# Kernel tuning notes

Measured on AMD Instinct MI355X. Metric: run time of the kernel, lower is better.

## Reference

```python
import jax, jax.numpy as jnp
import numpy as np

B, S, IN, H, L, HEM, HTR = 128, 256, 88, 400, 100, 100, 200


def _lin(x, W, b):
    return x @ W.T + b


def setup_inputs() -> dict:
    key = jax.random.key(0)
    ks = iter(jax.random.split(key, 64))
    def p(shape, scale=0.05):
        return jax.random.normal(next(ks), shape, dtype=jnp.float32) * scale
    inp = {
        "x": jax.random.uniform(next(ks), (B, S, IN), dtype=jnp.float32),
        # bidirectional tanh RNN (1 layer)
        "Wih_f": p((H, IN)), "Whh_f": p((H, H)), "bih_f": p((H,)), "bhh_f": p((H,)),
        "Wih_b": p((H, IN)), "Whh_b": p((H, H)), "bih_b": p((H,)), "bhh_b": p((H,)),
        # DKS combiner
        "Wc": p((H, L)), "bc": p((H,)),
        "Wmu": p((L, H)), "bmu": p((L,)),
        "Wsig": p((L, H)), "bsig": p((L,)),
        # emission MLP
        "We1": p((HEM, L)), "be1": p((HEM,)),
        "We2": p((HEM, HEM)), "be2": p((HEM,)),
        "We3": p((IN, HEM)), "be3": p((IN,)),
        # gate G
        "Wg1": p((HTR, L)), "bg1": p((HTR,)),
        "Wg2": p((L, HTR)), "bg2": p((L,)),
        # proposed mean H
        "Wh1": p((HTR, L)), "bh1": p((HTR,)),
        "Wh2": p((L, HTR)), "bh2": p((L,)),
        # gated linear mu (init: identity weight, zero bias)
        "Wmg": jnp.eye(L, dtype=jnp.float32), "bmg": jnp.zeros((L,), jnp.float32),
        "Wsg": p((L, L)), "bsg": p((L,)),
        # pre-drawn sampling noise (stands in for torch.randn_like)
        "noise_inf": jax.random.normal(next(ks), (S, B, L), dtype=jnp.float32),
        "z0_gen": jax.random.normal(next(ks), (B, L), dtype=jnp.float32),
        "noise_gen": jax.random.normal(next(ks), (S, B, L), dtype=jnp.float32),
    }
    return inp


def _forward(x, Wih_f, Whh_f, bih_f, bhh_f, Wih_b, Whh_b, bih_b, bhh_b,
             Wc, bc, Wmu, bmu, Wsig, bsig,
             We1, be1, We2, be2, We3, be3,
             Wg1, bg1, Wg2, bg2, Wh1, bh1, Wh2, bh2, Wmg, bmg, Wsg, bsg,
             noise_inf, z0_gen, noise_gen):
    Bs = x.shape[0]
    # ---- bidirectional tanh RNN (batch_first) ----
    xf = (x @ Wih_f.T + bih_f).transpose(1, 0, 2)  # [S,B,H]
    xb = (x @ Wih_b.T + bih_b).transpose(1, 0, 2)

    def rnn_step_f(h, xt):
        h = jnp.tanh(xt + h @ Whh_f.T + bhh_f)
        return h, h

    def rnn_step_b(h, xt):
        h = jnp.tanh(xt + h @ Whh_b.T + bhh_b)
        return h, h

    h0 = jnp.zeros((Bs, H), x.dtype)
    _, out_f = jax.lax.scan(rnn_step_f, h0, xf)                 # [S,B,H] forward dir
    _, out_b_rev = jax.lax.scan(rnn_step_b, h0, xb[::-1])       # backward dir
    h_right = out_b_rev[::-1]                                   # [S,B,H], time-aligned
    # (h_left = out_f unused for combiner_type='dks')

    # ---- DKS combiner: sequential latent sampling ----
    def comb_step(z_prev, inp):
        hr_t, n_t = inp
        h = 0.5 * (jnp.tanh(z_prev @ Wc.T + bc) + hr_t)
        mu = h @ Wmu.T + bmu
        var = jax.nn.softplus(h @ Wsig.T + bsig)
        z_t = mu + jnp.sqrt(var) * n_t
        return z_t, (z_t, mu, var)

    z0 = jnp.zeros((Bs, L), x.dtype)
    _, (Z, mus_inf, sigmas_inf) = jax.lax.scan(comb_step, z0, (h_right, noise_inf))
    Z = Z.transpose(1, 0, 2)                 # [B,S,L]
    mus_inf = mus_inf.transpose(1, 0, 2)
    sigmas_inf = sigmas_inf.transpose(1, 0, 2)

    # ---- decoder emission (vectorized over B,S) ----
    e = jax.nn.relu(_lin(Z, We1, be1))
    e = jax.nn.relu(_lin(e, We2, be2))
    x_hat = jax.nn.sigmoid(_lin(e, We3, be3))  # [B,S,IN]

    # ---- decoder transition prior (sequential, self-driven) ----
    def tr_step(z_prev, n_t):
        g = jax.nn.sigmoid(jax.nn.relu(z_prev @ Wg1.T + bg1) @ Wg2.T + bg2)
        h_prop = jax.nn.relu(z_prev @ Wh1.T + bh1) @ Wh2.T + bh2
        mu = h_prop * g + (z_prev @ Wmg.T + bmg) * (1.0 - g)
        sigma = jax.nn.softplus(jax.nn.relu(h_prop) @ Wsg.T + bsg)
        z_t = mu + jnp.sqrt(sigma) * n_t
        return z_t, (mu, sigma)

    _, (mus_gen, sigmas_gen) = jax.lax.scan(tr_step, z0_gen, noise_gen)
    mus_gen = mus_gen.transpose(1, 0, 2)
    sigmas_gen = sigmas_gen.transpose(1, 0, 2)

    return (x_hat, mus_inf, sigmas_inf, mus_gen, sigmas_gen)


def reference(x, Wih_f, Whh_f, bih_f, bhh_f, Wih_b, Whh_b, bih_b, bhh_b,
              Wc, bc, Wmu, bmu, Wsig, bsig,
              We1, be1, We2, be2, We3, be3,
              Wg1, bg1, Wg2, bg2, Wh1, bh1, Wh2, bh2, Wmg, bmg, Wsg, bsg,
              noise_inf, z0_gen, noise_gen):
    return _forward(x, Wih_f, Whh_f, bih_f, bhh_f, Wih_b, Whh_b, bih_b, bhh_b,
                    Wc, bc, Wmu, bmu, Wsig, bsig,
                    We1, be1, We2, be2, We3, be3,
                    Wg1, bg1, Wg2, bg2, Wh1, bh1, Wh2, bh2, Wmg, bmg, Wsg, bsg,
                    noise_inf, z0_gen, noise_gen)
```

## Files before the change

### kernel.cpp

```cpp
#include <hip/hip_runtime.h>
#include <math.h>

typedef float f32x4 __attribute__((ext_vector_type(4)));
typedef short s16x8 __attribute__((ext_vector_type(8)));
typedef unsigned short u16;

#define DI __device__ __forceinline__

DI float bf2f(u16 h) { union { unsigned u; float f; } v; v.u = ((unsigned)h) << 16; return v.f; }
DI u16 f2bf(float f) {
  union { float f; unsigned u; } v; v.f = f;
  unsigned u = v.u;
  u += 0x7FFFu + ((u >> 16) & 1u);
  return (u16)(u >> 16);
}
DI float tanh_fast(float x) {
  float e = __expf(2.f * x);
  return 1.f - 2.f / (e + 1.f);
}
DI float sigmoid_f(float x) { return 1.f / (1.f + __expf(-x)); }
DI float softplus_f(float x) { return fmaxf(x, 0.f) + log1pf(__expf(-fabsf(x))); }
DI f32x4 mfma16(s16x8 a, s16x8 b, f32x4 c) {
  return __builtin_amdgcn_mfma_f32_16x16x32_bf16(a, b, c, 0, 0, 0);
}
DI void bar_lds() { asm volatile("s_waitcnt lgkmcnt(0)\n\ts_barrier" ::: "memory"); }
DI int fa(int k, int row) { return ((k >> 5) << 9) + ((((k >> 3) & 3) * 16 + row) << 3) + (k & 7); }

union P16 { uint4 v[2]; u16 u[16]; };

static constexpr size_t U_RNN = 0;
static constexpr size_t U_C1  = 186368;
static constexpr size_t U_C2  = 243712;
static constexpr size_t U_GA  = 336896;
static constexpr size_t U_GB  = 394240;
static constexpr size_t U_GC  = 444416;
static constexpr size_t U_E1  = 473088;
static constexpr size_t U_E2  = 487424;
static constexpr size_t U_E3  = 501760;
static constexpr size_t U_IN  = 514048;
static constexpr size_t U_SL  = 552448;

__global__ void k_pack(u16* __restrict__ ws,
    const float* __restrict__ Whh_b, const float* __restrict__ Wc,
    const float* __restrict__ Wmu, const float* __restrict__ Wsig,
    const float* __restrict__ Wg1, const float* __restrict__ Wh1,
    const float* __restrict__ Wg2, const float* __restrict__ Wh2,
    const float* __restrict__ Wmg, const float* __restrict__ Wsg,
    const float* __restrict__ We1, const float* __restrict__ We2,
    const float* __restrict__ We3, const float* __restrict__ Wih_b)
{
  int r = blockIdx.x, l = threadIdx.x;
  int region, local;
  if      (r < 364)  { region = 0; local = r; }
  else if (r < 476)  { region = 1; local = r - 364; }
  else if (r < 658)  { region = 2; local = r - 476; }
  else if (r < 770)  { region = 3; local = r - 658; }
  else if (r < 868)  { region = 4; local = r - 770; }
  else if (r < 924)  { region = 5; local = r - 868; }
  else if (r < 952)  { region = 6; local = r - 924; }
  else if (r < 980)  { region = 7; local = r - 952; }
  else if (r < 1004) { region = 8; local = r - 980; }
  else               { region = 9; local = r - 1004; }

  int NT; size_t base;
  switch (region) {
    case 0: NT = 28; base = U_RNN; break;
    case 1: NT = 28; base = U_C1;  break;
    case 2: NT = 14; base = U_C2;  break;
    case 3: NT = 28; base = U_GA;  break;
    case 4: NT = 14; base = U_GB;  break;
    case 5: NT = 14; base = U_GC;  break;
    case 6: NT = 7;  base = U_E1;  break;
    case 7: NT = 7;  base = U_E2;  break;
    case 8: NT = 6;  base = U_E3;  break;
    default:NT = 25; base = U_IN;  break;
  }
  int kt = local / NT, nt = local % NT;
  u16* out = ws + base + ((size_t)local * 64 + l) * 8;
  #pragma unroll
  for (int e = 0; e < 8; ++e) {
    int k = kt * 32 + (l >> 4) * 8 + e;
    int n = nt * 16 + (l & 15);
    float v = 0.f;
    switch (region) {
      case 0: if (n < 400 && k < 400) v = Whh_b[n * 400 + k]; break;
      case 1: if (n < 400 && k < 100) v = Wc[n * 100 + k]; break;
      case 2: if (n < 112) { if (n < 100 && k < 400) v = Wmu[n * 400 + k]; }
              else { int m = n - 112; if (m < 100 && k < 400) v = Wsig[m * 400 + k]; } break;
      case 3: if (n < 208) { if (n < 200 && k < 100) v = Wg1[n * 100 + k]; }
              else if (n < 416) { int m = n - 208; if (m < 200 && k < 100) v = Wh1[m * 100 + k]; } break;
      case 4: if (n < 112) { if (n < 100 && k < 200) v = Wg2[n * 200 + k]; }
              else { int m = n - 112; if (m < 100 && k < 200) v = Wh2[m * 200 + k]; } break;
      case 5: if (n < 112) { if (n < 100 && k < 100) v = Wmg[n * 100 + k]; }
              else { int m = n - 112; if (m < 100 && k < 100) v = Wsg[m * 100 + k]; } break;
      case 6: if (n < 100 && k < 100) v = We1[n * 100 + k]; break;
      case 7: if (n < 100 && k < 100) v = We2[n * 100 + k]; break;
      case 8: if (n < 88  && k < 100) v = We3[n * 100 + k]; break;
      default:if (n < 400 && k < 88)  v = Wih_b[n * 88 + k]; break;
    }
    out[e] = f2bf(v);
  }
}

__global__ __launch_bounds__(256) void k_proj(
    const float* __restrict__ x, const float* __restrict__ bih_b,
    const u16* __restrict__ pk_in, u16* __restrict__ slot)
{
  __shared__ __align__(16) u16 x_lds[16][104];
  const int tid = threadIdx.x;
  const int cblk = blockIdx.x;
  const int b = cblk >> 4, s0 = (cblk & 15) << 4;
  const float* xg = x + (size_t)cblk * 16 * 88;
  for (int idx = tid; idx < 16 * 104; idx += 256) {
    int r = idx / 104, k = idx % 104;
    x_lds[r][k] = (k < 88) ? f2bf(xg[r * 88 + k]) : (u16)0;
  }
  __syncthreads();
  const int w = tid >> 6, l = tid & 63, g = l >> 4, li = l & 15;
  const int bid2 = b >> 4, r2 = b & 15, g2 = r2 >> 2, q2 = r2 & 3;
  s16x8 a[3];
  #pragma unroll
  for (int kt = 0; kt < 3; ++kt)
    a[kt] = *(const s16x8*)&x_lds[li][kt * 32 + g * 8];
  for (int nt = w; nt < 25; nt += 4) {
    f32x4 acc = (f32x4){0.f, 0.f, 0.f, 0.f};
    #pragma unroll
    for (int kt = 0; kt < 3; ++kt) {
      s16x8 bfr = *(const s16x8*)(pk_in + ((size_t)(kt * 25 + nt) * 64 + l) * 8);
      acc = mfma16(a[kt], bfr, acc);
    }
    int i = nt * 16 + li;
    float bias = bih_b[i];
    int thr = ((i >> 6) << 6) + (g2 << 4) + (i & 15);
    int elem = (((i >> 4) & 3) << 2) + q2;
    #pragma unroll
    for (int q = 0; q < 4; ++q) {
      int s = s0 + g * 4 + q;
      slot[((size_t)(s * 8 + bid2) * 448 + thr) * 16 + elem] = f2bf(acc[q] + bias);
    }
  }
}

__global__ __launch_bounds__(448) void k_scan(
    const u16* __restrict__ pk_rnn, const u16* __restrict__ pk_c1, const u16* __restrict__ pk_c2,
    const u16* __restrict__ pk_gA, const u16* __restrict__ pk_gB, const u16* __restrict__ pk_gC,
    u16* __restrict__ slot, const float* __restrict__ bhh_b,
    const float* __restrict__ bc, const float* __restrict__ bmu, const float* __restrict__ bsig,
    const float* __restrict__ noise_inf,
    const float* __restrict__ z0g, const float* __restrict__ bg1, const float* __restrict__ bh1,
    const float* __restrict__ bg2, const float* __restrict__ bh2,
    const float* __restrict__ bmg, const float* __restrict__ bsg,
    const float* __restrict__ noise_gen,
    float* __restrict__ mui, float* __restrict__ sgi,
    float* __restrict__ mug, float* __restrict__ sgg)
{
  __shared__ __align__(16) u16 sm[56320];
  const int tid = threadIdx.x;
  const int w = tid >> 6, l = tid & 63, g = l >> 4, li = l & 15;
  const int bid = blockIdx.x;

  {
    uint4 z4 = (uint4){0, 0, 0, 0};
    uint4* p = (uint4*)sm;
    for (int idx = tid; idx < 7040; idx += 448) p[idx] = z4;
  }
  __syncthreads();

  if (bid < 8) {
    const int b0 = bid * 16;
    {
      u16* slab = sm;
      u16* hbuf = sm + 43008;
      {
        const uint4* src = (const uint4*)(pk_rnn + (size_t)10 * 28 * 512);
        uint4* dst = (uint4*)slab;
        for (int idx = tid; idx < 5376; idx += 448) dst[idx] = src[idx];
      }
      s16x8 wf[4][10];
      #pragma unroll
      for (int nt_l = 0; nt_l < 4; ++nt_l) {
        int nt = w * 4 + nt_l;
        #pragma unroll
        for (int kt = 0; kt < 10; ++kt)
          wf[nt_l][kt] = *(const s16x8*)(pk_rnn + ((size_t)(kt * 28 + nt) * 64 + l) * 8);
      }
      bool nv[4]; float bias_r[4];
      #pragma unroll
      for (int nt_l = 0; nt_l < 4; ++nt_l) {
        int n = (w * 4 + nt_l) * 16 + li;
        nv[nt_l] = (n < 400);
        bias_r[nt_l] = nv[nt_l] ? bhh_b[n] : 0.f;
      }
      P16 pf;
      {
        size_t base = ((size_t)(255 * 8 + bid) * 448 + w * 64 + l) * 16;
        pf.v[0] = *(const uint4*)(slot + base);
        pf.v[1] = *(const uint4*)(slot + base + 8);
      }
      __syncthreads();
      int cur = 0;
      for (int t = 0; t < 256; ++t) {
        const int tt = 255 - t;
        f32x4 acc[4];
        #pragma unroll
        for (int i = 0; i < 4; ++i) acc[i] = (f32x4){0.f, 0.f, 0.f, 0.f};
        const u16* hb = hbuf + cur * 6656;
        #pragma unroll
        for (int kt = 0; kt < 13; ++kt) {
          s16x8 a = *(const s16x8*)(hb + kt * 512 + l * 8);
          if (kt < 10) {
            #pragma unroll
            for (int nt_l = 0; nt_l < 4; ++nt_l) acc[nt_l] = mfma16(a, wf[nt_l][kt], acc[nt_l]);
          } else {
            #pragma unroll
            for (int nt_l = 0; nt_l < 4; ++nt_l) {
              s16x8 bfr = *(const s16x8*)(slab + ((size_t)((kt - 10) * 28 + w * 4 + nt_l) * 512) + l * 8);
              acc[nt_l] = mfma16(a, bfr, acc[nt_l]);
            }
          }
        }
        u16* hn = hbuf + (cur ^ 1) * 6656;
        P16 st; st.v[0] = (uint4){0,0,0,0}; st.v[1] = (uint4){0,0,0,0};
        #pragma unroll
        for (int nt_l = 0; nt_l < 4; ++nt_l) {
          if (nv[nt_l]) {
            int n = (w * 4 + nt_l) * 16 + li;
            #pragma unroll
            for (int q = 0; q < 4; ++q) {
              float v = acc[nt_l][q] + bf2f(pf.u[nt_l * 4 + q]) + bias_r[nt_l];
              u16 hv = f2bf(tanh_fast(v));
              hn[fa(n, 4 * g + q)] = hv;
              st.u[nt_l * 4 + q] = hv;
            }
          }
        }
        {
          size_t base = ((size_t)(tt * 8 + bid) * 448 + w * 64 + l) * 16;
          *(uint4*)(slot + base) = st.v[0];
          *(uint4*)(slot + base + 8) = st.v[1];
        }
        if (t < 255) {
          size_t nb = ((size_t)((tt - 1) * 8 + bid) * 448 + w * 64 + l) * 16;
          pf.v[0] = *(const uint4*)(slot + nb);
          pf.v[1] = *(const uint4*)(slot + nb + 8);
        }
        bar_lds();
        cur ^= 1;
      }
    }
    __syncthreads();
    {
      u16* hbF = sm;
      u16* zbF = sm + 6656;
      for (int idx = tid; idx < 8704; idx += 448) sm[idx] = 0;
      s16x8 wC1[4][4], wMu[13], wSg[13];
      #pragma unroll
      for (int nt_l = 0; nt_l < 4; ++nt_l) {
        int nt = w * 4 + nt_l;
        #pragma unroll
        for (int kt = 0; kt < 4; ++kt)
          wC1[nt_l][kt] = *(const s16x8*)(pk_c1 + ((size_t)(kt * 28 + nt) * 64 + l) * 8);
      }
      #pragma unroll
      for (int kt = 0; kt < 13; ++kt) {
        wMu[kt] = *(const s16x8*)(pk_c2 + ((size_t)(kt * 14 + w) * 64 + l) * 8);
        wSg[kt] = *(const s16x8*)(pk_c2 + ((size_t)(kt * 14 + 7 + w) * 64 + l) * 8);
      }
      const int c = w * 16 + li;
      const bool cv = (c < 100);
      const float bmu_c = cv ? bmu[c] : 0.f;
      const float bsig_c = cv ? bsig[c] : 0.f;
      bool nv[4]; float bc_r[4];
      #pragma unroll
      for (int nt_l = 0; nt_l < 4; ++nt_l) {
        int n = (w * 4 + nt_l) * 16 + li;
        nv[nt_l] = (n < 400);
        bc_r[nt_l] = nv[nt_l] ? bc[n] : 0.f;
      }
      P16 pf;
      {
        size_t base = ((size_t)(0 * 8 + bid) * 448 + w * 64 + l) * 16;
        pf.v[0] = *(const uint4*)(slot + base);
        pf.v[1] = *(const uint4*)(slot + base + 8);
      }
      float pf_nz[4];
      #pragma unroll
      for (int q = 0; q < 4; ++q)
        pf_nz[q] = cv ? noise_inf[((size_t)0 * 128 + b0 + g * 4 + q) * 100 + c] : 0.f;
      __syncthreads();

      for (int t = 0; t < 256; ++t) {
        {
          s16x8 az[4];
          #pragma unroll
          for (int kt = 0; kt < 4; ++kt)
            az[kt] = *(const s16x8*)(zbF + kt * 512 + l * 8);
          f32x4 a1[4];
          #pragma unroll
          for (int i = 0; i < 4; ++i) a1[i] = (f32x4){0.f, 0.f, 0.f, 0.f};
          #pragma unroll
          for (int kt = 0; kt < 4; ++kt) {
            #pragma unroll
            for (int nt_l = 0; nt_l < 4; ++nt_l) a1[nt_l] = mfma16(az[kt], wC1[nt_l][kt], a1[nt_l]);
          }
          #pragma unroll
          for (int nt_l = 0; nt_l < 4; ++nt_l) {
            if (nv[nt_l]) {
              int n = (w * 4 + nt_l) * 16 + li;
              #pragma unroll
              for (int q = 0; q < 4; ++q) {
                float hv = 0.5f * (tanh_fast(a1[nt_l][q] + bc_r[nt_l]) + bf2f(pf.u[nt_l * 4 + q]));
                hbF[fa(n, 4 * g + q)] = f2bf(hv);
              }
            }
          }
          if (t < 255) {
            size_t nb = ((size_t)((t + 1) * 8 + bid) * 448 + w * 64 + l) * 16;
            pf.v[0] = *(const uint4*)(slot + nb);
            pf.v[1] = *(const uint4*)(slot + nb + 8);
          }
        }
        bar_lds();
        {
          f32x4 am = (f32x4){0.f,0.f,0.f,0.f}, as_ = am;
          #pragma unroll
          for (int kt = 0; kt < 13; ++kt) {
            s16x8 a = *(const s16x8*)(hbF + kt * 512 + l * 8);
            am = mfma16(a, wMu[kt], am);
            as_ = mfma16(a, wSg[kt], as_);
          }
          #pragma unroll
          for (int q = 0; q < 4; ++q) {
            int r = g * 4 + q;
            float mu = am[q] + bmu_c;
            float va = softplus_f(as_[q] + bsig_c);
            if (cv) {
              size_t o = ((size_t)(b0 + r) * 256 + t) * 100 + c;
              mui[o] = mu;
              sgi[o] = va;
              float z = mu + sqrtf(va) * pf_nz[q];
              zbF[fa(c, r)] = f2bf(z);
              slot[(size_t)(t * 8 + bid) * 7168 + r * 112 + c] = f2bf(z);
            }
          }
          if (t < 255) {
            #pragma unroll
            for (int q = 0; q < 4; ++q)
              if (cv) pf_nz[q] = noise_inf[((size_t)(t + 1) * 128 + b0 + g * 4 + q) * 100 + c];
          }
        }
        bar_lds();
      }
    }
  } else {
    const int b0 = (bid - 8) * 16;
    u16* zbF  = sm;
    u16* rhbF = sm + 2048;
    u16* t1F  = sm + 4096;
    u16* t2F  = sm + 7680;
    for (int idx = tid; idx < 2048; idx += 448) {
      int r = idx >> 7, c = idx & 127;
      zbF[fa(c, r)] = (c < 100) ? f2bf(z0g[(b0 + r) * 100 + c]) : (u16)0;
    }
    s16x8 wA[4][4], wBg[7], wBh[7], wCm[4], wCs[4];
    #pragma unroll
    for (int nt_l = 0; nt_l < 4; ++nt_l) {
      int nt = w * 4 + nt_l;
      #pragma unroll
      for (int kt = 0; kt < 4; ++kt)
        wA[nt_l][kt] = *(const s16x8*)(pk_gA + ((size_t)(kt * 28 + nt) * 64 + l) * 8);
    }
    #pragma unroll
    for (int kt = 0; kt < 7; ++kt) {
      wBg[kt] = *(const s16x8*)(pk_gB + ((size_t)(kt * 14 + w) * 64 + l) * 8);
      wBh[kt] = *(const s16x8*)(pk_gB + ((size_t)(kt * 14 + 7 + w) * 64 + l) * 8);
    }
    #pragma unroll
    for (int kt = 0; kt < 4; ++kt) {
      wCm[kt] = *(const s16x8*)(pk_gC + ((size_t)(kt * 14 + w) * 64 + l) * 8);
      wCs[kt] = *(const s16x8*)(pk_gC + ((size_t)(kt * 14 + 7 + w) * 64 + l) * 8);
    }
    const int c = w * 16 + li;
    const bool cv = (c < 100);
    const float bg2_c = cv ? bg2[c] : 0.f;
    const float bh2_c = cv ? bh2[c] : 0.f;
    const float bmg_c = cv ? bmg[c] : 0.f;
    const float bsg_c = cv ? bsg[c] : 0.f;
    float b1r[4];
    #pragma unroll
    for (int nt_l = 0; nt_l < 4; ++nt_l) {
      int n = (w * 4 + nt_l) * 16 + li;
      bool is1 = n < 208;
      int j = is1 ? n : n - 208;
      b1r[nt_l] = (n < 416 && j < 200) ? (is1 ? bg1[j] : bh1[j]) : 0.f;
    }
    float pfn[4];
    #pragma unroll
    for (int q = 0; q < 4; ++q)
      pfn[q] = cv ? noise_gen[((size_t)0 * 128 + b0 + g * 4 + q) * 100 + c] : 0.f;
    __syncthreads();

    for (int t = 0; t < 256; ++t) {
      s16x8 az[4];
      #pragma unroll
      for (int kt = 0; kt < 4; ++kt)
        az[kt] = *(const s16x8*)(zbF + kt * 512 + l * 8);
      {
        f32x4 a1[4];
        #pragma unroll
        for (int i = 0; i < 4; ++i) a1[i] = (f32x4){0.f, 0.f, 0.f, 0.f};
        #pragma unroll
        for (int kt = 0; kt < 4; ++kt) {
          #pragma unroll
          for (int nt_l = 0; nt_l < 4; ++nt_l) a1[nt_l] = mfma16(az[kt], wA[nt_l][kt], a1[nt_l]);
        }
        #pragma unroll
        for (int nt_l = 0; nt_l < 4; ++nt_l) {
          int n = (w * 4 + nt_l) * 16 + li;
          if (n < 416) {
            bool is1 = n < 208;
            int j = is1 ? n : n - 208;
            u16* dst = is1 ? t1F : t2F;
            #pragma unroll
            for (int q = 0; q < 4; ++q)
              dst[fa(j, 4 * g + q)] = f2bf(fmaxf(a1[nt_l][q] + b1r[nt_l], 0.f));
          }
        }
      }
      bar_lds();
      float muq[4];
      {
        f32x4 ag = (f32x4){0.f,0.f,0.f,0.f}, ah = ag, am = ag;
        #pragma unroll
        for (int kt = 0; kt < 7; ++kt) {
          s16x8 x1 = *(const s16x8*)(t1F + kt * 512 + l * 8);
          ag = mfma16(x1, wBg[kt], ag);
        }
        #pragma unroll
        for (int kt = 0; kt < 7; ++kt) {
          s16x8 x2 = *(const s16x8*)(t2F + kt * 512 + l * 8);
          ah = mfma16(x2, wBh[kt], ah);
        }
        #pragma unroll
        for (int kt = 0; kt < 4; ++kt) am = mfma16(az[kt], wCm[kt], am);
        #pragma unroll
        for (int q = 0; q < 4; ++q) {
          int r = g * 4 + q;
          float gv = sigmoid_f(ag[q] + bg2_c);
          float hp = ah[q] + bh2_c;
          float m0 = am[q] + bmg_c;
          muq[q] = hp * gv + m0 * (1.f - gv);
          rhbF[fa(c, r)] = f2bf(fmaxf(hp, 0.f));
          if (cv) mug[((size_t)(b0 + r) * 256 + t) * 100 + c] = muq[q];
        }
      }
      bar_lds();
      {
        f32x4 as2 = (f32x4){0.f,0.f,0.f,0.f};
        #pragma unroll
        for (int kt = 0; kt < 4; ++kt) {
          s16x8 xr = *(const s16x8*)(rhbF + kt * 512 + l * 8);
          as2 = mfma16(xr, wCs[kt], as2);
        }
        #pragma unroll
        for (int q = 0; q < 4; ++q) {
          int r = g * 4 + q;
          float sg = softplus_f(as2[q] + bsg_c);
          if (cv) {
            sgg[((size_t)(b0 + r) * 256 + t) * 100 + c] = sg;
            zbF[fa(c, r)] = f2bf(muq[q] + sqrtf(sg) * pfn[q]);
          }
        }
        if (t < 255) {
          #pragma unroll
          for (int q = 0; q < 4; ++q)
            if (cv) pfn[q] = noise_gen[((size_t)(t + 1) * 128 + b0 + g * 4 + q) * 100 + c];
        }
      }
      bar_lds();
    }
  }
}

__global__ __launch_bounds__(448) void k_dec(
    const u16* __restrict__ slot,
    const u16* __restrict__ pk_e1, const u16* __restrict__ pk_e2, const u16* __restrict__ pk_e3,
    const float* __restrict__ be1, const float* __restrict__ be2, const float* __restrict__ be3,
    float* __restrict__ xh)
{
  __shared__ __align__(16) u16 sm[3 * 2176];
  u16* zb = sm; u16* e1b = sm + 2176; u16* e2b = sm + 4352;
  const int tid = threadIdx.x;
  const int w = tid >> 6, l = tid & 63, g = l >> 4, li = l & 15;
  const int cc = blockIdx.x;
  const int b = cc >> 4, s0 = (cc & 15) << 4;
  const int bid2 = b >> 4, r2 = b & 15;

  s16x8 w1[4], w2[4], w3[4];
  #pragma unroll
  for (int kt = 0; kt < 4; ++kt) {
    w1[kt] = *(const s16x8*)(pk_e1 + ((size_t)(kt * 7 + w) * 64 + l) * 8);
    w2[kt] = *(const s16x8*)(pk_e2 + ((size_t)(kt * 7 + w) * 64 + l) * 8);
    if (w < 6) w3[kt] = *(const s16x8*)(pk_e3 + ((size_t)(kt * 6 + w) * 64 + l) * 8);
  }
  {
    for (int idx = tid; idx < 224; idx += 448) {
      int r = idx / 14, cj = idx % 14;
      size_t src = ((size_t)((s0 + r) * 8 + bid2)) * 7168 + r2 * 112 + cj * 8;
      *(uint4*)(zb + r * 136 + cj * 8) = *(const uint4*)(slot + src);
    }
    for (int idx = tid; idx < 3 * 384; idx += 448) {
      int bi = idx / 384, j = idx % 384;
      (sm + bi * 2176)[(j / 24) * 136 + 112 + (j % 24)] = 0;
    }
  }
  __syncthreads();
  const int c = w * 16 + li;
  {
    f32x4 acc = (f32x4){0.f,0.f,0.f,0.f};
    #pragma unroll
    for (int kt = 0; kt < 4; ++kt) {
      s16x8 a = *(const s16x8*)(zb + li * 136 + kt * 32 + g * 8);
      acc = mfma16(a, w1[kt], acc);
    }
    float bias = (c < 100) ? be1[c] : 0.f;
    #pragma unroll
    for (int q = 0; q < 4; ++q)
      e1b[(g * 4 + q) * 136 + c] = f2bf(fmaxf(acc[q] + bias, 0.f));
  }
  bar_lds();
  {
    f32x4 acc = (f32x4){0.f,0.f,0.f,0.f};
    #pragma unroll
    for (int kt = 0; kt < 4; ++kt) {
      s16x8 a = *(const s16x8*)(e1b + li * 136 + kt * 32 + g * 8);
      acc = mfma16(a, w2[kt], acc);
    }
    float bias = (c < 100) ? be2[c] : 0.f;
    #pragma unroll
    for (int q = 0; q < 4; ++q)
      e2b[(g * 4 + q) * 136 + c] = f2bf(fmaxf(acc[q] + bias, 0.f));
  }
  bar_lds();
  if (w < 6) {
    f32x4 acc = (f32x4){0.f,0.f,0.f,0.f};
    #pragma unroll
    for (int kt = 0; kt < 4; ++kt) {
      s16x8 a = *(const s16x8*)(e2b + li * 136 + kt * 32 + g * 8);
      acc = mfma16(a, w3[kt], acc);
    }
    int n = w * 16 + li;
    if (n < 88) {
      float bias = be3[n];
      #pragma unroll
      for (int q = 0; q < 4; ++q)
        xh[((size_t)b * 256 + s0 + g * 4 + q) * 88 + n] = sigmoid_f(acc[q] + bias);
    }
  }
}

extern "C" void kernel_launch(void* const* d_in, const int* in_sizes, int n_in,
                              void* d_out, int out_size, void* d_ws, size_t ws_size,
                              hipStream_t stream) {
  const float* x      = (const float*)d_in[0];
  const float* Wih_b  = (const float*)d_in[5];
  const float* Whh_b  = (const float*)d_in[6];
  const float* bih_b  = (const float*)d_in[7];
  const float* bhh_b  = (const float*)d_in[8];
  const float* Wc     = (const float*)d_in[9];
  const float* bc     = (const float*)d_in[10];
  const float* Wmu    = (const float*)d_in[11];
  const float* bmu    = (const float*)d_in[12];
  const float* Wsig   = (const float*)d_in[13];
  const float* bsig   = (const float*)d_in[14];
  const float* We1    = (const float*)d_in[15];
  const float* be1    = (const float*)d_in[16];
  const float* We2    = (const float*)d_in[17];
  const float* be2    = (const float*)d_in[18];
  const float* We3    = (const float*)d_in[19];
  const float* be3    = (const float*)d_in[20];
  const float* Wg1    = (const float*)d_in[21];
  const float* bg1    = (const float*)d_in[22];
  const float* Wg2    = (const float*)d_in[23];
  const float* bg2    = (const float*)d_in[24];
  const float* Wh1    = (const float*)d_in[25];
  const float* bh1    = (const float*)d_in[26];
  const float* Wh2    = (const float*)d_in[27];
  const float* bh2    = (const float*)d_in[28];
  const float* Wmg    = (const float*)d_in[29];
  const float* bmg    = (const float*)d_in[30];
  const float* Wsg    = (const float*)d_in[31];
  const float* bsg    = (const float*)d_in[32];
  const float* noise_inf = (const float*)d_in[33];
  const float* z0_gen    = (const float*)d_in[34];
  const float* noise_gen = (const float*)d_in[35];

  u16* ws16 = (u16*)d_ws;
  float* out = (float*)d_out;
  float* xh  = out;
  float* mui = out + 2883584;
  float* sgi = out + 6160384;
  float* mug = out + 9437184;
  float* sgg = out + 12713984;
  u16* slot = ws16 + U_SL;

  k_pack<<<1079, 64, 0, stream>>>(ws16, Whh_b, Wc, Wmu, Wsig, Wg1, Wh1, Wg2, Wh2,
                                  Wmg, Wsg, We1, We2, We3, Wih_b);
  k_proj<<<2048, 256, 0, stream>>>(x, bih_b, ws16 + U_IN, slot);
  k_scan<<<16, 448, 0, stream>>>(ws16 + U_RNN, ws16 + U_C1, ws16 + U_C2,
                                 ws16 + U_GA, ws16 + U_GB, ws16 + U_GC,
                                 slot, bhh_b,
                                 bc, bmu, bsig, noise_inf,
                                 z0_gen, bg1, bh1, bg2, bh2, bmg, bsg, noise_gen,
                                 mui, sgi, mug, sgg);
  k_dec<<<2048, 448, 0, stream>>>(slot, ws16 + U_E1, ws16 + U_E2, ws16 + U_E3,
                                  be1, be2, be3, xh);
}
```

Before: 1.775 ms.

## Hold full backward RNN weights in registers and skip padded MFMA tiles

The backward RNN scan now keeps all 13 K-tiles of its recurrent weight in registers instead of staging the last three tiles in an LDS slab. That removes per-step LDS weight reads and shrinks shared memory from about 110KB to 32KB. MFMAs and weight loads are also skipped for column tiles that are pure padding (beyond 25 or 26 tiles). The LDS hidden-state write is moved after the global slot store. The catch is much higher register pressure, roughly 208 VGPRs for the weight fragments alone, which could cause spills.

Measured after the change: 4.252 ms. 2.4x slower.

```diff
diff --git a/kernel.cpp b/kernel.cpp
--- a/kernel.cpp
+++ b/kernel.cpp
@@ -154,7 +154,7 @@
     float* __restrict__ mui, float* __restrict__ sgi,
     float* __restrict__ mug, float* __restrict__ sgg)
 {
-  __shared__ __align__(16) u16 sm[56320];
+  __shared__ __align__(16) u16 sm[16384];
   const int tid = threadIdx.x;
   const int w = tid >> 6, l = tid & 63, g = l >> 4, li = l & 15;
   const int bid = blockIdx.x;
@@ -162,34 +162,29 @@
   {
     uint4 z4 = (uint4){0, 0, 0, 0};
     uint4* p = (uint4*)sm;
-    for (int idx = tid; idx < 7040; idx += 448) p[idx] = z4;
+    for (int idx = tid; idx < 2048; idx += 448) p[idx] = z4;
   }
   __syncthreads();
 
   if (bid < 8) {
     const int b0 = bid * 16;
     {
-      u16* slab = sm;
-      u16* hbuf = sm + 43008;
-      {
-        const uint4* src = (const uint4*)(pk_rnn + (size_t)10 * 28 * 512);
-        uint4* dst = (uint4*)slab;
-        for (int idx = tid; idx < 5376; idx += 448) dst[idx] = src[idx];
-      }
-      s16x8 wf[4][10];
+      u16* hbuf = sm;
+      s16x8 wf[4][13];
       #pragma unroll
       for (int nt_l = 0; nt_l < 4; ++nt_l) {
         int nt = w * 4 + nt_l;
-        #pragma unroll
-        for (int kt = 0; kt < 10; ++kt)
-          wf[nt_l][kt] = *(const s16x8*)(pk_rnn + ((size_t)(kt * 28 + nt) * 64 + l) * 8);
-      }
-      bool nv[4]; float bias_r[4];
+        if (nt < 25) {
+          #pragma unroll
+          for (int kt = 0; kt < 13; ++kt)
+            wf[nt_l][kt] = *(const s16x8*)(pk_rnn + ((size_t)(kt * 28 + nt) * 64 + l) * 8);
+        }
+      }
+      float bias_r[4];
       #pragma unroll
       for (int nt_l = 0; nt_l < 4; ++nt_l) {
-        int n = (w * 4 + nt_l) * 16 + li;
-        nv[nt_l] = (n < 400);
-        bias_r[nt_l] = nv[nt_l] ? bhh_b[n] : 0.f;
+        int nt = w * 4 + nt_l;
+        bias_r[nt_l] = (nt < 25) ? bhh_b[nt * 16 + li] : 0.f;
       }
       P16 pf;
       {
@@ -208,29 +203,18 @@
         #pragma unroll
         for (int kt = 0; kt < 13; ++kt) {
           s16x8 a = *(const s16x8*)(hb + kt * 512 + l * 8);
-          if (kt < 10) {
-            #pragma unroll
-            for (int nt_l = 0; nt_l < 4; ++nt_l) acc[nt_l] = mfma16(a, wf[nt_l][kt], acc[nt_l]);
-          } else {
-            #pragma unroll
-            for (int nt_l = 0; nt_l < 4; ++nt_l) {
-              s16x8 bfr = *(const s16x8*)(slab + ((size_t)((kt - 10) * 28 + w * 4 + nt_l) * 512) + l * 8);
-              acc[nt_l] = mfma16(a, bfr, acc[nt_l]);
-            }
-          }
-        }
-        u16* hn = hbuf + (cur ^ 1) * 6656;
+          #pragma unroll
+          for (int nt_l = 0; nt_l < 4; ++nt_l)
+            if (w * 4 + nt_l < 25) acc[nt_l] = mfma16(a, wf[nt_l][kt], acc[nt_l]);
+        }
         P16 st; st.v[0] = (uint4){0,0,0,0}; st.v[1] = (uint4){0,0,0,0};
         #pragma unroll
         for (int nt_l = 0; nt_l < 4; ++nt_l) {
-          if (nv[nt_l]) {
-            int n = (w * 4 + nt_l) * 16 + li;
+          if (w * 4 + nt_l < 25) {
             #pragma unroll
             for (int q = 0; q < 4; ++q) {
               float v = acc[nt_l][q] + bf2f(pf.u[nt_l * 4 + q]) + bias_r[nt_l];
-              u16 hv = f2bf(tanh_fast(v));
-              hn[fa(n, 4 * g + q)] = hv;
-              st.u[nt_l * 4 + q] = hv;
+              st.u[nt_l * 4 + q] = f2bf(tanh_fast(v));
             }
           }
         }
@@ -238,6 +222,16 @@
           size_t base = ((size_t)(tt * 8 + bid) * 448 + w * 64 + l) * 16;
           *(uint4*)(slot + base) = st.v[0];
           *(uint4*)(slot + base + 8) = st.v[1];
+        }
+        u16* hn = hbuf + (cur ^ 1) * 6656;
+        #pragma unroll
+        for (int nt_l = 0; nt_l < 4; ++nt_l) {
+          if (w * 4 + nt_l < 25) {
+            int n = (w * 4 + nt_l) * 16 + li;
+            #pragma unroll
+            for (int q = 0; q < 4; ++q)
+              hn[fa(n, 4 * g + q)] = st.u[nt_l * 4 + q];
+          }
         }
         if (t < 255) {
           size_t nb = ((size_t)((tt - 1) * 8 + bid) * 448 + w * 64 + l) * 16;
@@ -257,9 +251,11 @@
       #pragma unroll
       for (int nt_l = 0; nt_l < 4; ++nt_l) {
         int nt = w * 4 + nt_l;
-        #pragma unroll
-        for (int kt = 0; kt < 4; ++kt)
-          wC1[nt_l][kt] = *(const s16x8*)(pk_c1 + ((size_t)(kt * 28 + nt) * 64 + l) * 8);
+        if (nt < 25) {
+          #pragma unroll
+          for (int kt = 0; kt < 4; ++kt)
+            wC1[nt_l][kt] = *(const s16x8*)(pk_c1 + ((size_t)(kt * 28 + nt) * 64 + l) * 8);
+        }
       }
       #pragma unroll
       for (int kt = 0; kt < 13; ++kt) {
@@ -270,12 +266,11 @@
       const bool cv = (c < 100);
       const float bmu_c = cv ? bmu[c] : 0.f;
       const float bsig_c = cv ? bsig[c] : 0.f;
-      bool nv[4]; float bc_r[4];
+      float bc_r[4];
       #pragma unroll
       for (int nt_l = 0; nt_l < 4; ++nt_l) {
-        int n = (w * 4 + nt_l) * 16 + li;
-        nv[nt_l] = (n < 400);
-        bc_r[nt_l] = nv[nt_l] ? bc[n] : 0.f;
+        int nt = w * 4 + nt_l;
+        bc_r[nt_l] = (nt < 25) ? bc[nt * 16 + li] : 0.f;
       }
       P16 pf;
       {
@@ -301,11 +296,12 @@
           #pragma unroll
           for (int kt = 0; kt < 4; ++kt) {
             #pragma unroll
-            for (int nt_l = 0; nt_l < 4; ++nt_l) a1[nt_l] = mfma16(az[kt], wC1[nt_l][kt], a1[nt_l]);
+            for (int nt_l = 0; nt_l < 4; ++nt_l)
+              if (w * 4 + nt_l < 25) a1[nt_l] = mfma16(az[kt], wC1[nt_l][kt], a1[nt_l]);
           }
           #pragma unroll
           for (int nt_l = 0; nt_l < 4; ++nt_l) {
-            if (nv[nt_l]) {
+            if (w * 4 + nt_l < 25) {
               int n = (w * 4 + nt_l) * 16 + li;
               #pragma unroll
               for (int q = 0; q < 4; ++q) {
@@ -366,9 +362,11 @@
     #pragma unroll
     for (int nt_l = 0; nt_l < 4; ++nt_l) {
       int nt = w * 4 + nt_l;
-      #pragma unroll
-      for (int kt = 0; kt < 4; ++kt)
-        wA[nt_l][kt] = *(const s16x8*)(pk_gA + ((size_t)(kt * 28 + nt) * 64 + l) * 8);
+      if (nt < 26) {
+        #pragma unroll
+        for (int kt = 0; kt < 4; ++kt)
+          wA[nt_l][kt] = *(const s16x8*)(pk_gA + ((size_t)(kt * 28 + nt) * 64 + l) * 8);
+      }
     }
     #pragma unroll
     for (int kt = 0; kt < 7; ++kt) {
@@ -412,7 +410,8 @@
         #pragma unroll
         for (int kt = 0; kt < 4; ++kt) {
           #pragma unroll
-          for (int nt_l = 0; nt_l < 4; ++nt_l) a1[nt_l] = mfma16(az[kt], wA[nt_l][kt], a1[nt_l]);
+          for (int nt_l = 0; nt_l < 4; ++nt_l)
+            if (w * 4 + nt_l < 26) a1[nt_l] = mfma16(az[kt], wA[nt_l][kt], a1[nt_l]);
         }
         #pragma unroll
         for (int nt_l = 0; nt_l < 4; ++nt_l) {
```

## Trim padded MFMA tiles in scan, fold RNN bias into projection, use packed bf16 converts

Applied to the files above, without the earlier changes.

Folds the bhh bias into the input projection kernel so the serial RNN step no longer adds it. In the recurrent scans, the last wave skips MFMA and epilogue work on padded output tiles (wave 6 handles one real tile instead of four; two in the gate stage). Float-to-bf16 rounding now uses the hardware v_cvt_pk_bf16_f32 instruction, and the RNN loop is unrolled by two so the ping-pong buffer pointers are fixed. These cut per-step latency on the serial critical path. The cost is extra code paths split by wave index, plus a possible small rounding difference from summing the two biases before the bf16 store.

After: 2.248 ms. 1.27x slower.

```diff
diff --git a/kernel.cpp b/kernel.cpp
--- a/kernel.cpp
+++ b/kernel.cpp
@@ -4,6 +4,7 @@
 typedef float f32x4 __attribute__((ext_vector_type(4)));
 typedef short s16x8 __attribute__((ext_vector_type(8)));
 typedef unsigned short u16;
+typedef unsigned int u32;
 
 #define DI __device__ __forceinline__
 
@@ -14,6 +15,11 @@
   u += 0x7FFFu + ((u >> 16) & 1u);
   return (u16)(u >> 16);
 }
+DI u32 cvt_pk(float lo, float hi) {
+  u32 r;
+  asm volatile("v_cvt_pk_bf16_f32 %0, %1, %2" : "=v"(r) : "v"(lo), "v"(hi));
+  return r;
+}
 DI float tanh_fast(float x) {
   float e = __expf(2.f * x);
   return 1.f - 2.f / (e + 1.f);
@@ -26,7 +32,7 @@
 DI void bar_lds() { asm volatile("s_waitcnt lgkmcnt(0)\n\ts_barrier" ::: "memory"); }
 DI int fa(int k, int row) { return ((k >> 5) << 9) + ((((k >> 3) & 3) * 16 + row) << 3) + (k & 7); }
 
-union P16 { uint4 v[2]; u16 u[16]; };
+union P16 { uint4 v[2]; u32 w32[8]; u16 u[16]; };
 
 static constexpr size_t U_RNN = 0;
 static constexpr size_t U_C1  = 186368;
@@ -103,7 +109,7 @@
 }
 
 __global__ __launch_bounds__(256) void k_proj(
-    const float* __restrict__ x, const float* __restrict__ bih_b,
+    const float* __restrict__ x, const float* __restrict__ bih_b, const float* __restrict__ bhh_b,
     const u16* __restrict__ pk_in, u16* __restrict__ slot)
 {
   __shared__ __align__(16) u16 x_lds[16][104];
@@ -130,7 +136,7 @@
       acc = mfma16(a[kt], bfr, acc);
     }
     int i = nt * 16 + li;
-    float bias = bih_b[i];
+    float bias = bih_b[i] + bhh_b[i];
     int thr = ((i >> 6) << 6) + (g2 << 4) + (i & 15);
     int elem = (((i >> 4) & 3) << 2) + q2;
     #pragma unroll
@@ -144,7 +150,7 @@
 __global__ __launch_bounds__(448) void k_scan(
     const u16* __restrict__ pk_rnn, const u16* __restrict__ pk_c1, const u16* __restrict__ pk_c2,
     const u16* __restrict__ pk_gA, const u16* __restrict__ pk_gB, const u16* __restrict__ pk_gC,
-    u16* __restrict__ slot, const float* __restrict__ bhh_b,
+    u16* __restrict__ slot,
     const float* __restrict__ bc, const float* __restrict__ bmu, const float* __restrict__ bsig,
     const float* __restrict__ noise_inf,
     const float* __restrict__ z0g, const float* __restrict__ bg1, const float* __restrict__ bh1,
@@ -184,13 +190,6 @@
         for (int kt = 0; kt < 10; ++kt)
           wf[nt_l][kt] = *(const s16x8*)(pk_rnn + ((size_t)(kt * 28 + nt) * 64 + l) * 8);
       }
-      bool nv[4]; float bias_r[4];
-      #pragma unroll
-      for (int nt_l = 0; nt_l < 4; ++nt_l) {
-        int n = (w * 4 + nt_l) * 16 + li;
-        nv[nt_l] = (n < 400);
-        bias_r[nt_l] = nv[nt_l] ? bhh_b[n] : 0.f;
-      }
       P16 pf;
       {
         size_t base = ((size_t)(255 * 8 + bid) * 448 + w * 64 + l) * 16;
@@ -198,54 +197,69 @@
         pf.v[1] = *(const uint4*)(slot + base + 8);
       }
       __syncthreads();
-      int cur = 0;
-      for (int t = 0; t < 256; ++t) {
+
+      auto step = [&](const u16* hb, u16* hn, int t) {
         const int tt = 255 - t;
         f32x4 acc[4];
         #pragma unroll
         for (int i = 0; i < 4; ++i) acc[i] = (f32x4){0.f, 0.f, 0.f, 0.f};
-        const u16* hb = hbuf + cur * 6656;
-        #pragma unroll
-        for (int kt = 0; kt < 13; ++kt) {
-          s16x8 a = *(const s16x8*)(hb + kt * 512 + l * 8);
-          if (kt < 10) {
-            #pragma unroll
-            for (int nt_l = 0; nt_l < 4; ++nt_l) acc[nt_l] = mfma16(a, wf[nt_l][kt], acc[nt_l]);
-          } else {
-            #pragma unroll
-            for (int nt_l = 0; nt_l < 4; ++nt_l) {
-              s16x8 bfr = *(const s16x8*)(slab + ((size_t)((kt - 10) * 28 + w * 4 + nt_l) * 512) + l * 8);
-              acc[nt_l] = mfma16(a, bfr, acc[nt_l]);
+        if (w < 6) {
+          #pragma unroll
+          for (int kt = 0; kt < 13; ++kt) {
+            s16x8 a = *(const s16x8*)(hb + kt * 512 + l * 8);
+            if (kt < 10) {
+              #pragma unroll
+              for (int nt_l = 0; nt_l < 4; ++nt_l) acc[nt_l] = mfma16(a, wf[nt_l][kt], acc[nt_l]);
+            } else {
+              #pragma unroll
+              for (int nt_l = 0; nt_l < 4; ++nt_l) {
+                s16x8 bfr = *(const s16x8*)(slab + ((size_t)((kt - 10) * 28 + w * 4 + nt_l) * 512) + l * 8);
+                acc[nt_l] = mfma16(a, bfr, acc[nt_l]);
+              }
             }
           }
-        }
-        u16* hn = hbuf + (cur ^ 1) * 6656;
+        } else {
+          #pragma unroll
+          for (int kt = 0; kt < 13; ++kt) {
+            s16x8 a = *(const s16x8*)(hb + kt * 512 + l * 8);
+            if (kt < 10) acc[0] = mfma16(a, wf[0][kt], acc[0]);
+            else {
+              s16x8 bfr = *(const s16x8*)(slab + ((size_t)((kt - 10) * 28 + w * 4) * 512) + l * 8);
+              acc[0] = mfma16(a, bfr, acc[0]);
+            }
+          }
+        }
+        const int nvmax = (w < 6) ? 4 : 1;
         P16 st; st.v[0] = (uint4){0,0,0,0}; st.v[1] = (uint4){0,0,0,0};
-        #pragma unroll
-        for (int nt_l = 0; nt_l < 4; ++nt_l) {
-          if (nv[nt_l]) {
-            int n = (w * 4 + nt_l) * 16 + li;
-            #pragma unroll
-            for (int q = 0; q < 4; ++q) {
-              float v = acc[nt_l][q] + bf2f(pf.u[nt_l * 4 + q]) + bias_r[nt_l];
-              u16 hv = f2bf(tanh_fast(v));
-              hn[fa(n, 4 * g + q)] = hv;
-              st.u[nt_l * 4 + q] = hv;
-            }
-          }
+        for (int nt_l = 0; nt_l < nvmax; ++nt_l) {
+          float t0 = tanh_fast(acc[nt_l][0] + bf2f(pf.u[nt_l * 4 + 0]));
+          float t1 = tanh_fast(acc[nt_l][1] + bf2f(pf.u[nt_l * 4 + 1]));
+          float t2 = tanh_fast(acc[nt_l][2] + bf2f(pf.u[nt_l * 4 + 2]));
+          float t3 = tanh_fast(acc[nt_l][3] + bf2f(pf.u[nt_l * 4 + 3]));
+          st.w32[nt_l * 2]     = cvt_pk(t0, t1);
+          st.w32[nt_l * 2 + 1] = cvt_pk(t2, t3);
         }
         {
           size_t base = ((size_t)(tt * 8 + bid) * 448 + w * 64 + l) * 16;
           *(uint4*)(slot + base) = st.v[0];
           *(uint4*)(slot + base + 8) = st.v[1];
         }
+        for (int nt_l = 0; nt_l < nvmax; ++nt_l) {
+          int n = (w * 4 + nt_l) * 16 + li;
+          #pragma unroll
+          for (int q = 0; q < 4; ++q)
+            hn[fa(n, 4 * g + q)] = st.u[nt_l * 4 + q];
+        }
         if (t < 255) {
           size_t nb = ((size_t)((tt - 1) * 8 + bid) * 448 + w * 64 + l) * 16;
           pf.v[0] = *(const uint4*)(slot + nb);
           pf.v[1] = *(const uint4*)(slot + nb + 8);
         }
         bar_lds();
-        cur ^= 1;
+      };
+      for (int t = 0; t < 256; t += 2) {
+        step(hbuf, hbuf + 6656, t);
+        step(hbuf + 6656, hbuf, t + 1);
       }
     }
     __syncthreads();
@@ -270,12 +284,11 @@
       const bool cv = (c < 100);
       const float bmu_c = cv ? bmu[c] : 0.f;
       const float bsig_c = cv ? bsig[c] : 0.f;
-      bool nv[4]; float bc_r[4];
+      float bc_r[4];
       #pragma unroll
       for (int nt_l = 0; nt_l < 4; ++nt_l) {
-        int n = (w * 4 + nt_l) * 16 + li;
-        nv[nt_l] = (n < 400);
-        bc_r[nt_l] = nv[nt_l] ? bc[n] : 0.f;
+        int nt = w * 4 + nt_l;
+        bc_r[nt_l] = (nt < 25) ? bc[nt * 16 + li] : 0.f;
       }
       P16 pf;
       {
@@ -289,6 +302,7 @@
         pf_nz[q] = cv ? noise_inf[((size_t)0 * 128 + b0 + g * 4 + q) * 100 + c] : 0.f;
       __syncthreads();
 
+      const int nvmax = (w < 6) ? 4 : 1;
       for (int t = 0; t < 256; ++t) {
         {
           s16x8 az[4];
@@ -298,21 +312,27 @@
           f32x4 a1[4];
           #pragma unroll
           for (int i = 0; i < 4; ++i) a1[i] = (f32x4){0.f, 0.f, 0.f, 0.f};
-          #pragma unroll
-          for (int kt = 0; kt < 4; ++kt) {
+          if (w < 6) {
             #pragma unroll
-            for (int nt_l = 0; nt_l < 4; ++nt_l) a1[nt_l] = mfma16(az[kt], wC1[nt_l][kt], a1[nt_l]);
-          }
-          #pragma unroll
-          for (int nt_l = 0; nt_l < 4; ++nt_l) {
-            if (nv[nt_l]) {
-              int n = (w * 4 + nt_l) * 16 + li;
+            for (int kt = 0; kt < 4; ++kt) {
               #pragma unroll
-              for (int q = 0; q < 4; ++q) {
-                float hv = 0.5f * (tanh_fast(a1[nt_l][q] + bc_r[nt_l]) + bf2f(pf.u[nt_l * 4 + q]));
-                hbF[fa(n, 4 * g + q)] = f2bf(hv);
-              }
+              for (int nt_l = 0; nt_l < 4; ++nt_l) a1[nt_l] = mfma16(az[kt], wC1[nt_l][kt], a1[nt_l]);
             }
+          } else {
+            #pragma unroll
+            for (int kt = 0; kt < 4; ++kt) a1[0] = mfma16(az[kt], wC1[0][kt], a1[0]);
+          }
+          for (int nt_l = 0; nt_l < nvmax; ++nt_l) {
+            int n = (w * 4 + nt_l) * 16 + li;
+            float h0 = 0.5f * (tanh_fast(a1[nt_l][0] + bc_r[nt_l]) + bf2f(pf.u[nt_l * 4 + 0]));
+            float h1 = 0.5f * (tanh_fast(a1[nt_l][1] + bc_r[nt_l]) + bf2f(pf.u[nt_l * 4 + 1]));
+            float h2 = 0.5f * (tanh_fast(a1[nt_l][2] + bc_r[nt_l]) + bf2f(pf.u[nt_l * 4 + 2]));
+            float h3 = 0.5f * (tanh_fast(a1[nt_l][3] + bc_r[nt_l]) + bf2f(pf.u[nt_l * 4 + 3]));
+            u32 p01 = cvt_pk(h0, h1), p23 = cvt_pk(h2, h3);
+            hbF[fa(n, 4 * g + 0)] = (u16)p01;
+            hbF[fa(n, 4 * g + 1)] = (u16)(p01 >> 16);
+            hbF[fa(n, 4 * g + 2)] = (u16)p23;
+            hbF[fa(n, 4 * g + 3)] = (u16)(p23 >> 16);
           }
           if (t < 255) {
             size_t nb = ((size_t)((t + 1) * 8 + bid) * 448 + w * 64 + l) * 16;
@@ -329,18 +349,24 @@
             am = mfma16(a, wMu[kt], am);
             as_ = mfma16(a, wSg[kt], as_);
           }
-          #pragma unroll
-          for (int q = 0; q < 4; ++q) {
-            int r = g * 4 + q;
-            float mu = am[q] + bmu_c;
-            float va = softplus_f(as_[q] + bsig_c);
-            if (cv) {
+          if (cv) {
+            float mu[4], va[4], z[4];
+            #pragma unroll
+            for (int q = 0; q < 4; ++q) {
+              mu[q] = am[q] + bmu_c;
+              va[q] = softplus_f(as_[q] + bsig_c);
+              z[q] = mu[q] + sqrtf(va[q]) * pf_nz[q];
+            }
+            u32 p01 = cvt_pk(z[0], z[1]), p23 = cvt_pk(z[2], z[3]);
+            u16 zb16[4] = { (u16)p01, (u16)(p01 >> 16), (u16)p23, (u16)(p23 >> 16) };
+            #pragma unroll
+            for (int q = 0; q < 4; ++q) {
+              int r = g * 4 + q;
               size_t o = ((size_t)(b0 + r) * 256 + t) * 100 + c;
-              mui[o] = mu;
-              sgi[o] = va;
-              float z = mu + sqrtf(va) * pf_nz[q];
-              zbF[fa(c, r)] = f2bf(z);
-              slot[(size_t)(t * 8 + bid) * 7168 + r * 112 + c] = f2bf(z);
+              mui[o] = mu[q];
+              sgi[o] = va[q];
+              zbF[fa(c, r)] = zb16[q];
+              slot[(size_t)(t * 8 + bid) * 7168 + r * 112 + c] = zb16[q];
             }
           }
           if (t < 255) {
@@ -400,6 +426,7 @@
       pfn[q] = cv ? noise_gen[((size_t)0 * 128 + b0 + g * 4 + q) * 100 + c] : 0.f;
     __syncthreads();
 
+    const int nA = (w < 6) ? 4 : 2;
     for (int t = 0; t < 256; ++t) {
       s16x8 az[4];
       #pragma unroll
@@ -409,22 +436,33 @@
         f32x4 a1[4];
         #pragma unroll
         for (int i = 0; i < 4; ++i) a1[i] = (f32x4){0.f, 0.f, 0.f, 0.f};
-        #pragma unroll
-        for (int kt = 0; kt < 4; ++kt) {
-          #pragma unroll
-          for (int nt_l = 0; nt_l < 4; ++nt_l) a1[nt_l] = mfma16(az[kt], wA[nt_l][kt], a1[nt_l]);
-        }
-        #pragma unroll
-        for (int nt_l = 0; nt_l < 4; ++nt_l) {
+        if (w < 6) {
+          #pragma unroll
+          for (int kt = 0; kt < 4; ++kt) {
+            #pragma unroll
+            for (int nt_l = 0; nt_l < 4; ++nt_l) a1[nt_l] = mfma16(az[kt], wA[nt_l][kt], a1[nt_l]);
+          }
+        } else {
+          #pragma unroll
+          for (int kt = 0; kt < 4; ++kt) {
+            a1[0] = mfma16(az[kt], wA[0][kt], a1[0]);
+            a1[1] = mfma16(az[kt], wA[1][kt], a1[1]);
+          }
+        }
+        for (int nt_l = 0; nt_l < nA; ++nt_l) {
           int n = (w * 4 + nt_l) * 16 + li;
-          if (n < 416) {
-            bool is1 = n < 208;
-            int j = is1 ? n : n - 208;
-            u16* dst = is1 ? t1F : t2F;
-            #pragma unroll
-            for (int q = 0; q < 4; ++q)
-              dst[fa(j, 4 * g + q)] = f2bf(fmaxf(a1[nt_l][q] + b1r[nt_l], 0.f));
-          }
+          bool is1 = n < 208;
+          int j = is1 ? n : n - 208;
+          u16* dst = is1 ? t1F : t2F;
+          float v0 = fmaxf(a1[nt_l][0] + b1r[nt_l], 0.f);
+          float v1 = fmaxf(a1[nt_l][1] + b1r[nt_l], 0.f);
+          float v2 = fmaxf(a1[nt_l][2] + b1r[nt_l], 0.f);
+          float v3 = fmaxf(a1[nt_l][3] + b1r[nt_l], 0.f);
+          u32 p01 = cvt_pk(v0, v1), p23 = cvt_pk(v2, v3);
+          dst[fa(j, 4 * g + 0)] = (u16)p01;
+          dst[fa(j, 4 * g + 1)] = (u16)(p01 >> 16);
+          dst[fa(j, 4 * g + 2)] = (u16)p23;
+          dst[fa(j, 4 * g + 3)] = (u16)(p23 >> 16);
         }
       }
       bar_lds();
@@ -443,15 +481,24 @@
         }
         #pragma unroll
         for (int kt = 0; kt < 4; ++kt) am = mfma16(az[kt], wCm[kt], am);
+        float rh[4];
         #pragma unroll
         for (int q = 0; q < 4; ++q) {
-          int r = g * 4 + q;
           float gv = sigmoid_f(ag[q] + bg2_c);
           float hp = ah[q] + bh2_c;
           float m0 = am[q] + bmg_c;
           muq[q] = hp * gv + m0 * (1.f - gv);
-          rhbF[fa(c, r)] = f2bf(fmaxf(hp, 0.f));
-          if (cv) mug[((size_t)(b0 + r) * 256 + t) * 100 + c] = muq[q];
+          rh[q] = fmaxf(hp, 0.f);
+        }
+        u32 p01 = cvt_pk(rh[0], rh[1]), p23 = cvt_pk(rh[2], rh[3]);
+        rhbF[fa(c, 4 * g + 0)] = (u16)p01;
+        rhbF[fa(c, 4 * g + 1)] = (u16)(p01 >> 16);
+        rhbF[fa(c, 4 * g + 2)] = (u16)p23;
+        rhbF[fa(c, 4 * g + 3)] = (u16)(p23 >> 16);
+        if (cv) {
+          #pragma unroll
+          for (int q = 0; q < 4; ++q)
+            mug[((size_t)(b0 + g * 4 + q) * 256 + t) * 100 + c] = muq[q];
         }
       }
       bar_lds();
@@ -462,13 +509,20 @@
           s16x8 xr = *(const s16x8*)(rhbF + kt * 512 + l * 8);
           as2 = mfma16(xr, wCs[kt], as2);
         }
-        #pragma unroll
-        for (int q = 0; q < 4; ++q) {
-          int r = g * 4 + q;
-          float sg = softplus_f(as2[q] + bsg_c);
-          if (cv) {
-            sgg[((size_t)(b0 + r) * 256 + t) * 100 + c] = sg;
-            zbF[fa(c, r)] = f2bf(muq[q] + sqrtf(sg) * pfn[q]);
+        if (cv) {
+          float sg[4], z[4];
+          #pragma unroll
+          for (int q = 0; q < 4; ++q) {
+            sg[q] = softplus_f(as2[q] + bsg_c);
+            z[q] = muq[q] + sqrtf(sg[q]) * pfn[q];
+          }
+          u32 p01 = cvt_pk(z[0], z[1]), p23 = cvt_pk(z[2], z[3]);
+          u16 zb16[4] = { (u16)p01, (u16)(p01 >> 16), (u16)p23, (u16)(p23 >> 16) };
+          #pragma unroll
+          for (int q = 0; q < 4; ++q) {
+            int r = g * 4 + q;
+            sgg[((size_t)(b0 + r) * 256 + t) * 100 + c] = sg[q];
+            zbF[fa(c, r)] = zb16[q];
           }
         }
         if (t < 255) {
@@ -606,10 +660,10 @@
 
   k_pack<<<1079, 64, 0, stream>>>(ws16, Whh_b, Wc, Wmu, Wsig, Wg1, Wh1, Wg2, Wh2,
                                   Wmg, Wsg, We1, We2, We3, Wih_b);
-  k_proj<<<2048, 256, 0, stream>>>(x, bih_b, ws16 + U_IN, slot);
+  k_proj<<<2048, 256, 0, stream>>>(x, bih_b, bhh_b, ws16 + U_IN, slot);
   k_scan<<<16, 448, 0, stream>>>(ws16 + U_RNN, ws16 + U_C1, ws16 + U_C2,
                                  ws16 + U_GA, ws16 + U_GB, ws16 + U_GC,
-                                 slot, bhh_b,
+                                 slot,
                                  bc, bmu, bsig, noise_inf,
                                  z0_gen, bg1, bh1, bg2, bh2, bmg, bsg, noise_gen,
                                  mui, sgi, mug, sgg);
```
